# Kernel optimization log

Measured on AMD Instinct MI355X. Metric: run time of the kernel, lower is better.

The kernel has to match this reference:

```python
import jax, jax.numpy as jnp
import numpy as np

B, S, D, H, HD = 1, 2048, 3072, 24, 128
FFN = int(D / 3 * 8)  # 8192
ADALN = 256
NORM_EPS = 1e-6
QK_EPS = 1e-5
AXES_DIMS = (16, 56, 56)
AXES_LENS = (64, 128, 128)
THETA = 256.0


def rmsnorm(x, w, eps):
    var = jnp.mean(jnp.square(x), axis=-1, keepdims=True)
    return x * jax.lax.rsqrt(var + eps) * w


def apply_rope(x, cos, sin):
    # x: [B,S,H,HD]; cos/sin: [B,S,HD//2] (broadcast over heads, matching freqs_cis.unsqueeze(2))
    xr = x[..., 0::2]
    xi = x[..., 1::2]
    c = cos[:, :, None, :]
    s = sin[:, :, None, :]
    or_ = xr * c - xi * s
    oi_ = xr * s + xi * c
    return jnp.stack([or_, oi_], axis=-1).reshape(x.shape)


def rope_angles(ids):
    # ids: [B,S,3] int; returns angles [B,S,HD//2] concatenated per axis like RopeEmbedder
    parts = []
    for d, idx_axis in zip(AXES_DIMS, range(len(AXES_DIMS))):
        freqs = 1.0 / (THETA ** (jnp.arange(0, d, 2, dtype=jnp.float32) / d))  # [d/2]
        ang = ids[..., idx_axis].astype(jnp.float32)[..., None] * freqs  # [B,S,d/2]
        parts.append(ang)
    return jnp.concatenate(parts, axis=-1)  # [B,S,64]


def setup_inputs() -> dict:
    key = jax.random.key(0)
    ks = jax.random.split(key, 20)
    w = 0.02
    ids = jnp.concatenate([
        jax.random.randint(ks[15], (B, S, 1), 0, AXES_LENS[0]),
        jax.random.randint(ks[16], (B, S, 1), 0, AXES_LENS[1]),
        jax.random.randint(ks[17], (B, S, 1), 0, AXES_LENS[2]),
    ], axis=-1)
    return {
        "x": jax.random.normal(ks[0], (B, S, D), jnp.float32),
        "adaln_input": jax.random.normal(ks[1], (B, ADALN), jnp.float32),
        "attn_mask": jnp.ones((B, S), dtype=bool),
        "ids": ids,
        "attn_norm1_w": jnp.ones((D,), jnp.float32),
        "attn_norm2_w": jnp.ones((D,), jnp.float32),
        "ffn_norm1_w": jnp.ones((D,), jnp.float32),
        "ffn_norm2_w": jnp.ones((D,), jnp.float32),
        "norm_q_w": jnp.ones((HD,), jnp.float32),
        "norm_k_w": jnp.ones((HD,), jnp.float32),
        "wq": jax.random.normal(ks[2], (D, D), jnp.float32) * w,
        "wk": jax.random.normal(ks[3], (D, D), jnp.float32) * w,
        "wv": jax.random.normal(ks[4], (D, D), jnp.float32) * w,
        "wo": jax.random.normal(ks[5], (D, D), jnp.float32) * w,
        "w1": jax.random.normal(ks[6], (D, FFN), jnp.float32) * w,
        "w2": jax.random.normal(ks[7], (FFN, D), jnp.float32) * w,
        "w3": jax.random.normal(ks[8], (D, FFN), jnp.float32) * w,
        "adaln_w": jax.random.normal(ks[9], (ADALN, 4 * D), jnp.float32) * w,
        "adaln_b": jnp.zeros((4 * D,), jnp.float32),
    }


def block_forward(x, adaln_input, attn_mask, ids,
                  attn_norm1_w, attn_norm2_w, ffn_norm1_w, ffn_norm2_w,
                  norm_q_w, norm_k_w, wq, wk, wv, wo, w1, w2, w3,
                  adaln_w, adaln_b):
    ang = rope_angles(ids)
    cos, sin = jnp.cos(ang), jnp.sin(ang)

    mod = adaln_input @ adaln_w + adaln_b
    scale_msa, gate_msa, scale_mlp, gate_mlp = jnp.split(mod[:, None, :], 4, axis=2)
    gate_msa, gate_mlp = jnp.tanh(gate_msa), jnp.tanh(gate_mlp)
    scale_msa, scale_mlp = 1.0 + scale_msa, 1.0 + scale_mlp

    # Attention branch
    xs = rmsnorm(x, attn_norm1_w, NORM_EPS) * scale_msa  # [B,S,D]
    q = (xs @ wq).reshape(B, S, H, HD)
    k = (xs @ wk).reshape(B, S, H, HD)
    v = (xs @ wv).reshape(B, S, H, HD)
    q = rmsnorm(q, norm_q_w, QK_EPS)
    k = rmsnorm(k, norm_k_w, QK_EPS)
    q = apply_rope(q, cos, sin)
    k = apply_rope(k, cos, sin)

    scores = jnp.einsum('bqhd,bkhd->bhqk', q, k) / jnp.sqrt(jnp.float32(HD))
    neg = jnp.finfo(scores.dtype).min
    scores = jnp.where(attn_mask[:, None, None, :], scores, neg)
    probs = jax.nn.softmax(scores, axis=-1)
    attn = jnp.einsum('bhqk,bkhd->bqhd', probs, v).reshape(B, S, D)
    attn_out = attn @ wo

    x = x + gate_msa * rmsnorm(attn_out, attn_norm2_w, NORM_EPS)

    # FFN branch (SwiGLU)
    xf = rmsnorm(x, ffn_norm1_w, NORM_EPS) * scale_mlp
    h = jax.nn.silu(xf @ w1) * (xf @ w3)
    ffn_out = h @ w2
    x = x + gate_mlp * rmsnorm(ffn_out, ffn_norm2_w, NORM_EPS)
    return x


def reference(x, adaln_input, attn_mask, ids,
              attn_norm1_w, attn_norm2_w, ffn_norm1_w, ffn_norm2_w,
              norm_q_w, norm_k_w, wq, wk, wv, wo, w1, w2, w3,
              adaln_w, adaln_b):
    return block_forward(x, adaln_input, attn_mask, ids,
                         attn_norm1_w, attn_norm2_w, ffn_norm1_w, ffn_norm2_w,
                         norm_q_w, norm_k_w, wq, wk, wv, wo, w1, w2, w3,
                         adaln_w, adaln_b)
```

## Files before the change

kernel.cpp:

```cpp
#include <hip/hip_runtime.h>

#define AS1 __attribute__((address_space(1)))
#define AS3 __attribute__((address_space(3)))

typedef __bf16 bf16;
using bf16x8 = __attribute__((ext_vector_type(8))) __bf16;
using bf16x4 = __attribute__((ext_vector_type(4))) __bf16;
using bf16x2 = __attribute__((ext_vector_type(2))) __bf16;
using f32x4  = __attribute__((ext_vector_type(4))) float;


__device__ inline float wsum(float v) {
#pragma unroll
  for (int o = 32; o; o >>= 1) v += __shfl_xor(v, o, 64);
  return v;
}

template <int EPI>
__global__ __launch_bounds__(512, 1) void gemm256(
    const bf16* __restrict__ A, const bf16* __restrict__ Bt, void* __restrict__ Cv,
    int K, int lda, int ldb, int ldc, long long kOff, long long sC) {
  __shared__ bf16 lds[2][2][256 * 64];
  const int t = threadIdx.x;
  const int lane = t & 63, wid = t >> 6;
  const int wm = wid >> 2, wn = wid & 3;
  const int row16 = lane & 15, kg = lane >> 4;
  const int m0 = blockIdx.x * 256, n0 = blockIdx.y * 256;
  const int NT = K >> 6;
  const int sgran = (lane & 7) ^ (lane >> 3);
  A += (long long)blockIdx.z * kOff;
  Bt += (long long)blockIdx.z * kOff;

  auto stageA = [&](int buf, int r, int tk) {
    const int wrow = ((wid & 4) << 5) + (r << 5) + ((wid & 3) << 3);
    __builtin_amdgcn_global_load_lds(
        (const AS1 void*)(A + (long long)(m0 + wrow + (lane >> 3)) * lda + tk * 64 +
                          (sgran << 3)),
        (AS3 void*)&lds[buf][0][wrow * 64], 16, 0, 0);
  };
  auto stageB = [&](int buf, int r, int tk) {
    const int wrow = ((wid & 4) << 5) + (r << 5) + ((wid & 3) << 3);
    __builtin_amdgcn_global_load_lds(
        (const AS1 void*)(Bt + (long long)(n0 + wrow + (lane >> 3)) * ldb + tk * 64 +
                          (sgran << 3)),
        (AS3 void*)&lds[buf][1][wrow * 64], 16, 0, 0);
  };

  f32x4 acc[8][4];
#pragma unroll
  for (int i = 0; i < 8; ++i)
#pragma unroll
    for (int j = 0; j < 4; ++j) acc[i][j] = (f32x4){0.f, 0.f, 0.f, 0.f};

#pragma unroll
  for (int r = 0; r < 4; ++r) { stageA(0, r, 0); stageB(0, r, 0); }
#pragma unroll
  for (int r = 0; r < 3; ++r) { stageA(1, r, 1); stageB(1, r, 1); }

  bf16x8 bfr[4][2], af[2][2];

  for (int kt = 0; kt < NT; ++kt) {
    const int cb = kt & 1, nb = cb ^ 1;
    if (kt + 1 < NT) asm volatile("s_waitcnt vmcnt(6)" ::: "memory");
    else             asm volatile("s_waitcnt vmcnt(0)" ::: "memory");
    __builtin_amdgcn_s_barrier();

    if (kt + 1 < NT) { stageA(nb, 3, kt + 1); stageB(nb, 3, kt + 1); }
#pragma unroll
    for (int ni = 0; ni < 4; ++ni)
#pragma unroll
      for (int kk = 0; kk < 2; ++kk) {
        const int r = wn * 64 + ni * 16 + row16;
        bfr[ni][kk] = *(const bf16x8*)&lds[cb][1][r * 64 + (((kk * 4 + kg) ^ (r & 7)) << 3)];
      }
#pragma unroll
    for (int mi = 0; mi < 2; ++mi)
#pragma unroll
      for (int kk = 0; kk < 2; ++kk) {
        const int r = wm * 128 + mi * 16 + row16;
        af[mi][kk] = *(const bf16x8*)&lds[cb][0][r * 64 + (((kk * 4 + kg) ^ (r & 7)) << 3)];
      }
    asm volatile("s_waitcnt lgkmcnt(0)" ::: "memory");
    __builtin_amdgcn_s_setprio(1);
#pragma unroll
    for (int kk = 0; kk < 2; ++kk)
#pragma unroll
      for (int mi = 0; mi < 2; ++mi)
#pragma unroll
        for (int ni = 0; ni < 4; ++ni)
          acc[mi][ni] =
              __builtin_amdgcn_mfma_f32_16x16x32_bf16(af[mi][kk], bfr[ni][kk], acc[mi][ni], 0, 0, 0);
    __builtin_amdgcn_s_setprio(0);

#pragma unroll
    for (int q = 1; q < 4; ++q) {
      __builtin_amdgcn_s_barrier();
      if (kt + 2 < NT) { stageA(cb, q - 1, kt + 2); stageB(cb, q - 1, kt + 2); }
#pragma unroll
      for (int mi = 0; mi < 2; ++mi)
#pragma unroll
        for (int kk = 0; kk < 2; ++kk) {
          const int r = wm * 128 + q * 32 + mi * 16 + row16;
          af[mi][kk] = *(const bf16x8*)&lds[cb][0][r * 64 + (((kk * 4 + kg) ^ (r & 7)) << 3)];
        }
      asm volatile("s_waitcnt lgkmcnt(0)" ::: "memory");
      __builtin_amdgcn_s_setprio(1);
#pragma unroll
      for (int kk = 0; kk < 2; ++kk)
#pragma unroll
        for (int mi = 0; mi < 2; ++mi)
#pragma unroll
          for (int ni = 0; ni < 4; ++ni)
            acc[q * 2 + mi][ni] = __builtin_amdgcn_mfma_f32_16x16x32_bf16(
                af[mi][kk], bfr[ni][kk], acc[q * 2 + mi][ni], 0, 0, 0);
      __builtin_amdgcn_s_setprio(0);
    }
  }

  float* Cf = (float*)Cv;
  bf16* Cb = (bf16*)Cv;
  const long long cz = (long long)blockIdx.z * sC;
#pragma unroll
  for (int mf = 0; mf < 8; ++mf)
#pragma unroll
    for (int ni = 0; ni < 4; ++ni)
#pragma unroll
      for (int rr = 0; rr < 4; ++rr) {
        const int row = m0 + wm * 128 + (mf >> 1) * 32 + (mf & 1) * 16 + kg * 4 + rr;
        const int col = n0 + wn * 64 + ni * 16 + row16;
        const long long idx = cz + (long long)row * ldc + col;
        const float v = acc[mf][ni][rr];
        if constexpr (EPI == 0) Cf[idx] = v;
        else Cb[idx] = (bf16)v;
      }
}

template <int EPI>
__global__ __launch_bounds__(512, 1) void gemm192(
    const bf16* __restrict__ A, const bf16* __restrict__ Bt, void* __restrict__ Cv,
    int K, int lda, int ldb, int ldc, long long kOff, long long sC) {
  __shared__ bf16 lds[2][448 * 64];
  const int t = threadIdx.x;
  const int lane = t & 63, wid = t >> 6;
  const int wm = wid >> 2, wn = wid & 3;
  const int row16 = lane & 15, kg = lane >> 4;
  const int m0 = blockIdx.x * 256, n0 = blockIdx.y * 192;
  const int NT = K >> 6;
  const int sgran = (lane & 7) ^ (lane >> 3);
  A += (long long)blockIdx.z * kOff;
  Bt += (long long)blockIdx.z * kOff;

  auto stageA = [&](int buf, int r, int tk) {
    const int wrow = ((wid & 4) << 5) + (r << 5) + ((wid & 3) << 3);
    __builtin_amdgcn_global_load_lds(
        (const AS1 void*)(A + (long long)(m0 + wrow + (lane >> 3)) * lda + tk * 64 +
                          (sgran << 3)),
        (AS3 void*)&lds[buf][wrow * 64], 16, 0, 0);
  };
  auto stageB = [&](int buf, int r, int tk) {
    const int wrow = r * 64 + wid * 8;
    __builtin_amdgcn_global_load_lds(
        (const AS1 void*)(Bt + (long long)(n0 + wrow + (lane >> 3)) * ldb + tk * 64 +
                          (sgran << 3)),
        (AS3 void*)&lds[buf][(256 + wrow) * 64], 16, 0, 0);
  };

  f32x4 acc[8][3];
#pragma unroll
  for (int i = 0; i < 8; ++i)
#pragma unroll
    for (int j = 0; j < 3; ++j) acc[i][j] = (f32x4){0.f, 0.f, 0.f, 0.f};

#pragma unroll
  for (int r = 0; r < 4; ++r) stageA(0, r, 0);
#pragma unroll
  for (int r = 0; r < 3; ++r) stageB(0, r, 0);
#pragma unroll
  for (int r = 0; r < 3; ++r) { stageA(1, r, 1); stageB(1, r, 1); }

  bf16x8 bfr[3][2], af[2][2];

  for (int kt = 0; kt < NT; ++kt) {
    const int cb = kt & 1, nb = cb ^ 1;
    if (kt + 1 < NT) asm volatile("s_waitcnt vmcnt(6)" ::: "memory");
    else             asm volatile("s_waitcnt vmcnt(0)" ::: "memory");
    __builtin_amdgcn_s_barrier();

    if (kt + 1 < NT) stageA(nb, 3, kt + 1);
#pragma unroll
    for (int ni = 0; ni < 3; ++ni)
#pragma unroll
      for (int kk = 0; kk < 2; ++kk) {
        const int r = wn * 48 + ni * 16 + row16;
        bfr[ni][kk] =
            *(const bf16x8*)&lds[cb][(256 + r) * 64 + (((kk * 4 + kg) ^ (r & 7)) << 3)];
      }
#pragma unroll
    for (int mi = 0; mi < 2; ++mi)
#pragma unroll
      for (int kk = 0; kk < 2; ++kk) {
        const int r = wm * 128 + mi * 16 + row16;
        af[mi][kk] = *(const bf16x8*)&lds[cb][r * 64 + (((kk * 4 + kg) ^ (r & 7)) << 3)];
      }
    __builtin_amdgcn_s_barrier();
    asm volatile("s_waitcnt lgkmcnt(0)" ::: "memory");
    __builtin_amdgcn_s_setprio(1);
#pragma unroll
    for (int kk = 0; kk < 2; ++kk)
#pragma unroll
      for (int mi = 0; mi < 2; ++mi)
#pragma unroll
        for (int ni = 0; ni < 3; ++ni)
          acc[mi][ni] =
              __builtin_amdgcn_mfma_f32_16x16x32_bf16(af[mi][kk], bfr[ni][kk], acc[mi][ni], 0, 0, 0);
    __builtin_amdgcn_s_setprio(0);

#pragma unroll
    for (int q = 1; q < 4; ++q) {
      __builtin_amdgcn_s_barrier();
      if (kt + 2 < NT) { stageA(cb, q - 1, kt + 2); stageB(cb, q - 1, kt + 2); }
#pragma unroll
      for (int mi = 0; mi < 2; ++mi)
#pragma unroll
        for (int kk = 0; kk < 2; ++kk) {
          const int r = wm * 128 + q * 32 + mi * 16 + row16;
          af[mi][kk] = *(const bf16x8*)&lds[cb][r * 64 + (((kk * 4 + kg) ^ (r & 7)) << 3)];
        }
      __builtin_amdgcn_s_barrier();
      asm volatile("s_waitcnt lgkmcnt(0)" ::: "memory");
      __builtin_amdgcn_s_setprio(1);
#pragma unroll
      for (int kk = 0; kk < 2; ++kk)
#pragma unroll
        for (int mi = 0; mi < 2; ++mi)
#pragma unroll
          for (int ni = 0; ni < 3; ++ni)
            acc[q * 2 + mi][ni] = __builtin_amdgcn_mfma_f32_16x16x32_bf16(
                af[mi][kk], bfr[ni][kk], acc[q * 2 + mi][ni], 0, 0, 0);
      __builtin_amdgcn_s_setprio(0);
    }
  }

  float* Cf = (float*)Cv;
  bf16* Cb = (bf16*)Cv;
  const long long cz = (long long)blockIdx.z * sC;
#pragma unroll
  for (int mf = 0; mf < 8; ++mf)
#pragma unroll
    for (int ni = 0; ni < 3; ++ni)
#pragma unroll
      for (int rr = 0; rr < 4; ++rr) {
        const int row = m0 + wm * 128 + (mf >> 1) * 32 + (mf & 1) * 16 + kg * 4 + rr;
        const int col = n0 + wn * 48 + ni * 16 + row16;
        const long long idx = cz + (long long)row * ldc + col;
        const float v = acc[mf][ni][rr];
        if constexpr (EPI == 0) Cf[idx] = v;
        else Cb[idx] = (bf16)v;
      }
}

__global__ __launch_bounds__(256) void flash_attn_k(const bf16* __restrict__ qkv,
                                                    const bf16* __restrict__ vt,
                                                    float* __restrict__ Op,
                                                    float* __restrict__ mlp) {
  __shared__ bf16 Ks[64 * 128];
  __shared__ bf16 Vs[128 * 64];
  __shared__ bf16 Ps[4 * 32 * 64];
  const int t = threadIdx.x, lane = t & 63, wid = t >> 6;
  const int row16 = lane & 15, kg = lane >> 4;
  const int q0 = blockIdx.x * 128;
  const int h = blockIdx.y;
  const int z = blockIdx.z;
  const bf16* Qp = qkv + h * 128;
  const bf16* Kp = qkv + 3072 + h * 128;
  const bf16* Vt = vt + (long long)h * 262144;
  const float iscale = 0.08838834764831845f;

  bf16x8 qf[2][4];
#pragma unroll
  for (int mi = 0; mi < 2; ++mi)
#pragma unroll
    for (int kc = 0; kc < 4; ++kc)
      qf[mi][kc] = *(const bf16x8*)&Qp[(long long)(q0 + wid * 32 + mi * 16 + row16) * 9216 +
                                       kc * 32 + kg * 8];
  bf16x8 ones;
#pragma unroll
  for (int j = 0; j < 8; ++j) ones[j] = (bf16)1.0f;

  f32x4 oacc[2][8];
#pragma unroll
  for (int mi = 0; mi < 2; ++mi)
#pragma unroll
    for (int nd = 0; nd < 8; ++nd) oacc[mi][nd] = (f32x4){0.f, 0.f, 0.f, 0.f};
  f32x4 lacc[2] = {(f32x4){0.f, 0.f, 0.f, 0.f}, (f32x4){0.f, 0.f, 0.f, 0.f}};
  float mst[2][4];
#pragma unroll
  for (int mi = 0; mi < 2; ++mi)
#pragma unroll
    for (int r = 0; r < 4; ++r) mst[mi][r] = -1e30f;

  bf16* Pw = &Ps[wid * 2048];
  const int kvbase = z << 10;

  for (int kv0 = kvbase; kv0 < kvbase + 1024; kv0 += 64) {
#pragma unroll
    for (int p = 0; p < 4; ++p) {
      const int gi = p * 256 + t;
      const int row = gi >> 4, g = gi & 15;
      __builtin_amdgcn_global_load_lds(
          (const AS1 void*)(Kp + (long long)(kv0 + row) * 9216 + ((g ^ (row & 7)) << 3)),
          (AS3 void*)&Ks[(p * 256 + wid * 64) * 8], 16, 0, 0);
    }
#pragma unroll
    for (int p = 0; p < 4; ++p) {
      const int gi = p * 256 + t;
      const int row = gi >> 3, g = gi & 7;
      __builtin_amdgcn_global_load_lds(
          (const AS1 void*)(Vt + (long long)row * 2048 + kv0 + ((g ^ (row & 7)) << 3)),
          (AS3 void*)&Vs[(p * 256 + wid * 64) * 8], 16, 0, 0);
    }
    __syncthreads();

    f32x4 sacc[2][4];
#pragma unroll
    for (int mi = 0; mi < 2; ++mi)
#pragma unroll
      for (int nf = 0; nf < 4; ++nf) sacc[mi][nf] = (f32x4){0.f, 0.f, 0.f, 0.f};
#pragma unroll
    for (int kc = 0; kc < 4; ++kc) {
      bf16x8 kf[4];
#pragma unroll
      for (int nf = 0; nf < 4; ++nf) {
        const int row = nf * 16 + row16;
        kf[nf] = *(const bf16x8*)&Ks[(row * 16 + ((kc * 4 + kg) ^ (row & 7))) * 8];
      }
#pragma unroll
      for (int mi = 0; mi < 2; ++mi)
#pragma unroll
        for (int nf = 0; nf < 4; ++nf)
          sacc[mi][nf] =
              __builtin_amdgcn_mfma_f32_16x16x32_bf16(qf[mi][kc], kf[nf], sacc[mi][nf], 0, 0, 0);
    }

    float fac[2][4];
#pragma unroll
    for (int mi = 0; mi < 2; ++mi)
#pragma unroll
      for (int r = 0; r < 4; ++r) {
        float rm = sacc[mi][0][r];
#pragma unroll
        for (int nf = 1; nf < 4; ++nf) rm = fmaxf(rm, sacc[mi][nf][r]);
        rm = fmaxf(rm, __shfl_xor(rm, 1, 64));
        rm = fmaxf(rm, __shfl_xor(rm, 2, 64));
        rm = fmaxf(rm, __shfl_xor(rm, 4, 64));
        rm = fmaxf(rm, __shfl_xor(rm, 8, 64));
        const float mnew = fmaxf(mst[mi][r], rm * iscale);
        fac[mi][r] = __expf(mst[mi][r] - mnew);
        mst[mi][r] = mnew;
#pragma unroll
        for (int nf = 0; nf < 4; ++nf)
          sacc[mi][nf][r] = __expf(sacc[mi][nf][r] * iscale - mnew);
      }
#pragma unroll
    for (int mi = 0; mi < 2; ++mi)
#pragma unroll
      for (int r = 0; r < 4; ++r) {
        lacc[mi][r] *= fac[mi][r];
#pragma unroll
        for (int nd = 0; nd < 8; ++nd) oacc[mi][nd][r] *= fac[mi][r];
      }

#pragma unroll
    for (int mi = 0; mi < 2; ++mi)
#pragma unroll
      for (int nf = 0; nf < 4; ++nf)
#pragma unroll
        for (int r = 0; r < 4; ++r) {
          const int row = mi * 16 + kg * 4 + r;
          const int col = nf * 16 + row16;
          Pw[(row * 8 + ((col >> 3) ^ (row & 7))) * 8 + (col & 7)] = (bf16)sacc[mi][nf][r];
        }

#pragma unroll
    for (int kvc = 0; kvc < 2; ++kvc) {
      bf16x8 pf[2], vf[8];
#pragma unroll
      for (int mi = 0; mi < 2; ++mi) {
        const int row = mi * 16 + row16;
        pf[mi] = *(const bf16x8*)&Pw[(row * 8 + ((kvc * 4 + kg) ^ (row & 7))) * 8];
      }
#pragma unroll
      for (int nd = 0; nd < 8; ++nd) {
        const int row = nd * 16 + row16;
        vf[nd] = *(const bf16x8*)&Vs[(row * 8 + ((kvc * 4 + kg) ^ (row & 7))) * 8];
      }
#pragma unroll
      for (int mi = 0; mi < 2; ++mi) {
        lacc[mi] = __builtin_amdgcn_mfma_f32_16x16x32_bf16(pf[mi], ones, lacc[mi], 0, 0, 0);
#pragma unroll
        for (int nd = 0; nd < 8; ++nd)
          oacc[mi][nd] =
              __builtin_amdgcn_mfma_f32_16x16x32_bf16(pf[mi], vf[nd], oacc[mi][nd], 0, 0, 0);
      }
    }
    __syncthreads();
  }

  float* Oz = Op + (long long)z * 6291456;
#pragma unroll
  for (int mi = 0; mi < 2; ++mi)
#pragma unroll
    for (int nd = 0; nd < 8; ++nd)
#pragma unroll
      for (int r = 0; r < 4; ++r) {
        const int row = q0 + wid * 32 + mi * 16 + kg * 4 + r;
        const int col = h * 128 + nd * 16 + row16;
        Oz[(long long)row * 3072 + col] = oacc[mi][nd][r];
      }
  if (row16 == 0) {
#pragma unroll
    for (int mi = 0; mi < 2; ++mi)
#pragma unroll
      for (int r = 0; r < 4; ++r) {
        const int s = q0 + wid * 32 + mi * 16 + kg * 4 + r;
        const long long mi2 = ((long long)z * 49152 + s * 24 + h) * 2;
        mlp[mi2] = mst[mi][r];
        mlp[mi2 + 1] = lacc[mi][r];
      }
  }
}

__global__ __launch_bounds__(256) void fa_combine_k(const float* __restrict__ Op,
                                                    const float* __restrict__ mlp,
                                                    bf16* __restrict__ attn) {
  const int t = threadIdx.x, lane = t & 63, wid = t >> 6;
  const int pair = blockIdx.x * 4 + wid;
  const int s = pair / 24, h = pair % 24;
  const float2 ml0 = *(const float2*)&mlp[(long long)pair * 2];
  const float2 ml1 = *(const float2*)&mlp[(49152LL + pair) * 2];
  const float m = fmaxf(ml0.x, ml1.x);
  const float a0 = __expf(ml0.x - m), a1 = __expf(ml1.x - m);
  const float inv = 1.f / (ml0.y * a0 + ml1.y * a1);
  const long long base = (long long)s * 3072 + h * 128 + lane * 2;
  const float2 o0 = *(const float2*)&Op[base];
  const float2 o1 = *(const float2*)&Op[6291456LL + base];
  bf16x2 o;
  o[0] = (bf16)((o0.x * a0 + o1.x * a1) * inv);
  o[1] = (bf16)((o0.y * a0 + o1.y * a1) * inv);
  *(bf16x2*)&attn[base] = o;
}

__device__ inline void convT_tile(const float* __restrict__ in, bf16* __restrict__ out,
                                  int R, int C, int bx, int by) {
  __shared__ float tile[64][65];
  const int t = threadIdx.x;
  const int r0 = by * 64, c0 = bx * 64;
#pragma unroll
  for (int it = 0; it < 4; ++it) {
    const int idx = it * 256 + t;
    const int rl = idx >> 4, c4 = (idx & 15) << 2;
    const float4 v = *(const float4*)&in[(long long)(r0 + rl) * C + c0 + c4];
    tile[rl][c4 + 0] = v.x;
    tile[rl][c4 + 1] = v.y;
    tile[rl][c4 + 2] = v.z;
    tile[rl][c4 + 3] = v.w;
  }
  __syncthreads();
#pragma unroll
  for (int it = 0; it < 4; ++it) {
    const int idx = it * 256 + t;
    const int cl = idx >> 4, r4 = (idx & 15) << 2;
    bf16x4 o;
    o[0] = (bf16)tile[r4 + 0][cl];
    o[1] = (bf16)tile[r4 + 1][cl];
    o[2] = (bf16)tile[r4 + 2][cl];
    o[3] = (bf16)tile[r4 + 3][cl];
    *(bf16x4*)&out[(long long)(c0 + cl) * R + r0 + r4] = o;
  }
}

__global__ __launch_bounds__(256) void convAll(
    const float* __restrict__ wq, const float* __restrict__ wk,
    const float* __restrict__ wv, const float* __restrict__ wo,
    const float* __restrict__ w1, const float* __restrict__ w3,
    const float* __restrict__ w2, bf16* __restrict__ wqkvT, bf16* __restrict__ woT,
    bf16* __restrict__ w13T, bf16* __restrict__ w2T) {
  const int id = blockIdx.x;
  if (id < 9216) {
    const int m = id / 2304, l = id % 2304;
    const float* in = m == 0 ? wq : m == 1 ? wk : m == 2 ? wv : wo;
    bf16* out = m < 3 ? wqkvT + (long long)m * 9437184 : woT;
    convT_tile(in, out, 3072, 3072, l % 48, l / 48);
  } else if (id < 21504) {
    int l = id - 9216;
    const int m = l / 6144;
    l %= 6144;
    convT_tile(m ? w3 : w1, w13T + (long long)m * 25165824, 3072, 8192, l % 128, l / 128);
  } else {
    const int l = id - 21504;
    convT_tile(w2, w2T, 8192, 3072, l % 48, l / 48);
  }
}

__global__ __launch_bounds__(256) void ropetab_k(const int* __restrict__ ids,
                                                 float* __restrict__ cosT,
                                                 float* __restrict__ sinT) {
  const int i = blockIdx.x * 256 + threadIdx.x;
  const int s = i >> 6, j = i & 63;
  int ax, fi;
  float d;
  if (j < 8) { ax = 0; fi = j; d = 16.f; }
  else if (j < 36) { ax = 1; fi = j - 8; d = 56.f; }
  else { ax = 2; fi = j - 36; d = 56.f; }
  const float freq = exp2f(-16.f * (float)fi / d);
  const float ang = (float)ids[s * 3 + ax] * freq;
  cosT[i] = cosf(ang);
  sinT[i] = sinf(ang);
}

__global__ __launch_bounds__(256) void adaln_kernel(const float* __restrict__ ain,
                                                    const float* __restrict__ W,
                                                    const float* __restrict__ b,
                                                    float* __restrict__ out) {
  __shared__ float a[256];
  const int t = threadIdx.x;
  a[t] = ain[t];
  __syncthreads();
  const int n = blockIdx.x * 256 + t;
  float acc = b[n];
  for (int k = 0; k < 256; ++k) acc = fmaf(a[k], W[(long long)k * 12288 + n], acc);
  const int chunk = n / 3072;
  out[n] = (chunk & 1) ? tanhf(acc) : (1.f + acc);
}

__global__ __launch_bounds__(256) void rmsnorm_scale_k(const float* __restrict__ x,
                                                       const float* __restrict__ w,
                                                       const float* __restrict__ scale,
                                                       bf16* __restrict__ out) {
  __shared__ float red[4];
  const int t = threadIdx.x, lane = t & 63, wid = t >> 6;
  const long long base = (long long)blockIdx.x * 3072;
  float v[12];
  float ss = 0.f;
#pragma unroll
  for (int ch = 0; ch < 3; ++ch) {
    const float4 f = *(const float4*)&x[base + ch * 1024 + t * 4];
    v[ch * 4 + 0] = f.x; v[ch * 4 + 1] = f.y; v[ch * 4 + 2] = f.z; v[ch * 4 + 3] = f.w;
    ss += f.x * f.x + f.y * f.y + f.z * f.z + f.w * f.w;
  }
  ss = wsum(ss);
  if (!lane) red[wid] = ss;
  __syncthreads();
  const float r = rsqrtf((red[0] + red[1] + red[2] + red[3]) / 3072.f + 1e-6f);
#pragma unroll
  for (int ch = 0; ch < 3; ++ch) {
    const int col = ch * 1024 + t * 4;
    bf16x4 o;
#pragma unroll
    for (int j = 0; j < 4; ++j) o[j] = (bf16)(v[ch * 4 + j] * r * w[col + j] * scale[col + j]);
    *(bf16x4*)&out[base + col] = o;
  }
}

__global__ __launch_bounds__(256) void qknorm_rope_k(bf16* __restrict__ qkv,
                                                     const float* __restrict__ cosT,
                                                     const float* __restrict__ sinT,
                                                     const float* __restrict__ wq,
                                                     const float* __restrict__ wk) {
  const int t = threadIdx.x, lane = t & 63, wid = t >> 6;
  const int idx = blockIdx.x * 4 + wid;
  const int s = idx / 24, h = idx % 24;
  const int isK = blockIdx.y;
  bf16* base = qkv + (long long)s * 9216 + isK * 3072 + h * 128;
  bf16x2 p = *(const bf16x2*)(base + 2 * lane);
  float xr = (float)p[0], xi = (float)p[1];
  const float ss = wsum(xr * xr + xi * xi);
  const float r = rsqrtf(ss / 128.f + 1e-5f);
  const float* w = isK ? wk : wq;
  const float2 wv = *(const float2*)&w[2 * lane];
  xr *= r * wv.x;
  xi *= r * wv.y;
  const float c = cosT[s * 64 + lane], sn = sinT[s * 64 + lane];
  bf16x2 o;
  o[0] = (bf16)(xr * c - xi * sn);
  o[1] = (bf16)(xr * sn + xi * c);
  *(bf16x2*)(base + 2 * lane) = o;
}

__global__ __launch_bounds__(256) void vtrans_k(const bf16* __restrict__ qkv,
                                                bf16* __restrict__ vt) {
  __shared__ bf16 tile[64][72];
  const int t = threadIdx.x;
  const int s0 = blockIdx.x * 64, d0 = blockIdx.y * 64, h = blockIdx.z;
#pragma unroll
  for (int it = 0; it < 2; ++it) {
    const int idx = it * 256 + t;
    const int sl = idx >> 3, c8 = (idx & 7) << 3;
    const bf16x8 v =
        *(const bf16x8*)&qkv[(long long)(s0 + sl) * 9216 + 6144 + h * 128 + d0 + c8];
    *(bf16x8*)&tile[sl][c8] = v;
  }
  __syncthreads();
#pragma unroll
  for (int it = 0; it < 2; ++it) {
    const int idx = it * 256 + t;
    const int dl = idx >> 3, s8 = (idx & 7) << 3;
    bf16x8 o;
#pragma unroll
    for (int j = 0; j < 8; ++j) o[j] = tile[s8 + j][dl];
    *(bf16x8*)&vt[(long long)h * 262144 + (long long)(d0 + dl) * 2048 + s0 + s8] = o;
  }
}

__global__ __launch_bounds__(256) void silumul_k(const bf16* __restrict__ t13,
                                                 bf16* __restrict__ h) {
  const int gi = blockIdx.x * 256 + threadIdx.x;
  const int s = gi >> 10, j8 = (gi & 1023) << 3;
  const bf16x8 a = *(const bf16x8*)&t13[(long long)s * 16384 + j8];
  const bf16x8 b = *(const bf16x8*)&t13[(long long)s * 16384 + 8192 + j8];
  bf16x8 o;
#pragma unroll
  for (int j = 0; j < 8; ++j) {
    const float x = (float)a[j];
    const float sl = x / (1.f + __expf(-x));
    o[j] = (bf16)(sl * (float)b[j]);
  }
  *(bf16x8*)&h[(long long)s * 8192 + j8] = o;
}

__global__ __launch_bounds__(256) void resid1_k(
    const float* __restrict__ x, const float* __restrict__ p0, const float* __restrict__ p1,
    const float* __restrict__ n2w, const float* __restrict__ gate,
    const float* __restrict__ f1w, const float* __restrict__ smlp,
    float* __restrict__ x1, bf16* __restrict__ xf) {
  __shared__ float red[8];
  const int t = threadIdx.x, lane = t & 63, wid = t >> 6;
  const long long base = (long long)blockIdx.x * 3072;
  float av[12];
  float ss = 0.f;
#pragma unroll
  for (int ch = 0; ch < 3; ++ch) {
    const float4 f0 = *(const float4*)&p0[base + ch * 1024 + t * 4];
    const float4 f1 = *(const float4*)&p1[base + ch * 1024 + t * 4];
    const float a0 = f0.x + f1.x, a1 = f0.y + f1.y, a2 = f0.z + f1.z, a3 = f0.w + f1.w;
    av[ch * 4 + 0] = a0; av[ch * 4 + 1] = a1; av[ch * 4 + 2] = a2; av[ch * 4 + 3] = a3;
    ss += a0 * a0 + a1 * a1 + a2 * a2 + a3 * a3;
  }
  ss = wsum(ss);
  if (!lane) red[wid] = ss;
  __syncthreads();
  const float r = rsqrtf((red[0] + red[1] + red[2] + red[3]) / 3072.f + 1e-6f);
  float xv[12];
  float ss2 = 0.f;
#pragma unroll
  for (int ch = 0; ch < 3; ++ch) {
    const int col = ch * 1024 + t * 4;
    const float4 f = *(const float4*)&x[base + col];
    float4 o;
    o.x = f.x + gate[col + 0] * (av[ch * 4 + 0] * r * n2w[col + 0]);
    o.y = f.y + gate[col + 1] * (av[ch * 4 + 1] * r * n2w[col + 1]);
    o.z = f.z + gate[col + 2] * (av[ch * 4 + 2] * r * n2w[col + 2]);
    o.w = f.w + gate[col + 3] * (av[ch * 4 + 3] * r * n2w[col + 3]);
    *(float4*)&x1[base + col] = o;
    xv[ch * 4 + 0] = o.x; xv[ch * 4 + 1] = o.y; xv[ch * 4 + 2] = o.z; xv[ch * 4 + 3] = o.w;
    ss2 += o.x * o.x + o.y * o.y + o.z * o.z + o.w * o.w;
  }
  ss2 = wsum(ss2);
  if (!lane) red[4 + wid] = ss2;
  __syncthreads();
  const float r2 = rsqrtf((red[4] + red[5] + red[6] + red[7]) / 3072.f + 1e-6f);
#pragma unroll
  for (int ch = 0; ch < 3; ++ch) {
    const int col = ch * 1024 + t * 4;
    bf16x4 o;
#pragma unroll
    for (int j = 0; j < 4; ++j)
      o[j] = (bf16)(xv[ch * 4 + j] * r2 * f1w[col + j] * smlp[col + j]);
    *(bf16x4*)&xf[base + col] = o;
  }
}

__global__ __launch_bounds__(256) void resid2_k(const float* __restrict__ x1,
                                                const float* __restrict__ f0,
                                                const float* __restrict__ f1,
                                                const float* __restrict__ nw,
                                                const float* __restrict__ gate,
                                                float* __restrict__ out) {
  __shared__ float red[4];
  const int t = threadIdx.x, lane = t & 63, wid = t >> 6;
  const long long base = (long long)blockIdx.x * 3072;
  float fv[12];
  float ss = 0.f;
#pragma unroll
  for (int ch = 0; ch < 3; ++ch) {
    const float4 a = *(const float4*)&f0[base + ch * 1024 + t * 4];
    const float4 b = *(const float4*)&f1[base + ch * 1024 + t * 4];
    const float a0 = a.x + b.x, a1 = a.y + b.y, a2 = a.z + b.z, a3 = a.w + b.w;
    fv[ch * 4 + 0] = a0; fv[ch * 4 + 1] = a1; fv[ch * 4 + 2] = a2; fv[ch * 4 + 3] = a3;
    ss += a0 * a0 + a1 * a1 + a2 * a2 + a3 * a3;
  }
  ss = wsum(ss);
  if (!lane) red[wid] = ss;
  __syncthreads();
  const float r = rsqrtf((red[0] + red[1] + red[2] + red[3]) / 3072.f + 1e-6f);
#pragma unroll
  for (int ch = 0; ch < 3; ++ch) {
    const int col = ch * 1024 + t * 4;
    const float4 f = *(const float4*)&x1[base + col];
    float4 o;
    o.x = f.x + gate[col + 0] * (fv[ch * 4 + 0] * r * nw[col + 0]);
    o.y = f.y + gate[col + 1] * (fv[ch * 4 + 1] * r * nw[col + 1]);
    o.z = f.z + gate[col + 2] * (fv[ch * 4 + 2] * r * nw[col + 2]);
    o.w = f.w + gate[col + 3] * (fv[ch * 4 + 3] * r * nw[col + 3]);
    *(float4*)&out[base + col] = o;
  }
}

extern "C" void kernel_launch(void* const* d_in, const int* in_sizes, int n_in,
                              void* d_out, int out_size, void* d_ws, size_t ws_size,
                              hipStream_t stream) {
  const float* x    = (const float*)d_in[0];
  const float* ain  = (const float*)d_in[1];
  const int* ids    = (const int*)d_in[3];
  const float* n1w  = (const float*)d_in[4];
  const float* n2w  = (const float*)d_in[5];
  const float* fn1w = (const float*)d_in[6];
  const float* fn2w = (const float*)d_in[7];
  const float* nqw  = (const float*)d_in[8];
  const float* nkw  = (const float*)d_in[9];
  const float* wq   = (const float*)d_in[10];
  const float* wk   = (const float*)d_in[11];
  const float* wv   = (const float*)d_in[12];
  const float* wo   = (const float*)d_in[13];
  const float* w1   = (const float*)d_in[14];
  const float* w2   = (const float*)d_in[15];
  const float* w3   = (const float*)d_in[16];
  const float* adw  = (const float*)d_in[17];
  const float* adb  = (const float*)d_in[18];

  if (ws_size < 395362304ULL) return;

  char* ws = (char*)d_ws;
  bf16* wqkvT = (bf16*)(ws + 0LL);
  bf16* woT   = (bf16*)(ws + 56623104LL);
  bf16* w13T  = (bf16*)(ws + 75497472LL);
  bf16* w2T   = (bf16*)(ws + 176160768LL);
  float* cosT = (float*)(ws + 226492416LL);
  float* sinT = (float*)(ws + 227016704LL);
  float* adv  = (float*)(ws + 227540992LL);
  bf16* xs    = (bf16*)(ws + 227590144LL);
  char* big   = ws + 240173056LL;
  float* x1   = (float*)(big);
  bf16* qkv   = (bf16*)(big + 25165824LL);
  bf16* vt    = (bf16*)(big + 62914560LL);
  bf16* attn  = (bf16*)(big + 75497472LL);
  float* aoP  = (float*)(big + 88080384LL);
  float* Opart= (float*)(big + 88080384LL);
  float* mlp  = (float*)(big + 138412032LL);
  bf16* t13   = (bf16*)(big + 25165824LL);
  bf16* hbuf  = (bf16*)(big + 92274688LL);
  float* ffnP = (float*)(big + 25165824LL);

  const dim3 b256(256);
  const dim3 b512(512);

  ropetab_k<<<dim3(512), b256, 0, stream>>>(ids, cosT, sinT);
  adaln_kernel<<<dim3(48), b256, 0, stream>>>(ain, adw, adb, adv);

  convAll<<<dim3(27648), b256, 0, stream>>>(wq, wk, wv, wo, w1, w3, w2, wqkvT, woT, w13T,
                                            w2T);

  rmsnorm_scale_k<<<dim3(2048), b256, 0, stream>>>(x, n1w, adv, xs);

  gemm192<1><<<dim3(8, 48, 1), b512, 0, stream>>>(xs, wqkvT, qkv, 3072, 3072, 3072, 9216,
                                                  0LL, 0LL);

  qknorm_rope_k<<<dim3(12288, 2), b256, 0, stream>>>(qkv, cosT, sinT, nqw, nkw);
  vtrans_k<<<dim3(32, 2, 24), b256, 0, stream>>>(qkv, vt);

  flash_attn_k<<<dim3(16, 24, 2), b256, 0, stream>>>(qkv, vt, Opart, mlp);
  fa_combine_k<<<dim3(12288), b256, 0, stream>>>(Opart, mlp, attn);

  gemm192<0><<<dim3(8, 16, 2), b512, 0, stream>>>(attn, woT, aoP, 1536, 3072, 3072, 3072,
                                                  1536LL, 6291456LL);
  resid1_k<<<dim3(2048), b256, 0, stream>>>(x, aoP, aoP + 6291456LL, n2w, adv + 3072, fn1w,
                                            adv + 6144, x1, xs);
  gemm256<1><<<dim3(8, 64, 1), b512, 0, stream>>>(xs, w13T, t13, 3072, 3072, 3072, 16384,
                                                  0LL, 0LL);
  silumul_k<<<dim3(8192), b256, 0, stream>>>(t13, hbuf);
  gemm192<0><<<dim3(8, 16, 2), b512, 0, stream>>>(hbuf, w2T, ffnP, 4096, 8192, 8192, 3072,
                                                  4096LL, 6291456LL);
  resid2_k<<<dim3(2048), b256, 0, stream>>>(x1, ffnP, ffnP + 6291456LL, fn2w, adv + 9216,
                                            (float*)d_out);
}
```

Measured before the change: 837.6 us.

## Fuse SwiGLU into W1/W3 GEMM epilogue and store attention partials as bf16

```diff
diff --git a/kernel.cpp b/kernel.cpp
--- a/kernel.cpp
+++ b/kernel.cpp
@@ -128,10 +128,18 @@
       for (int rr = 0; rr < 4; ++rr) {
         const int row = m0 + wm * 128 + (mf >> 1) * 32 + (mf & 1) * 16 + kg * 4 + rr;
         const int col = n0 + wn * 64 + ni * 16 + row16;
-        const long long idx = cz + (long long)row * ldc + col;
         const float v = acc[mf][ni][rr];
-        if constexpr (EPI == 0) Cf[idx] = v;
-        else Cb[idx] = (bf16)v;
+        if constexpr (EPI == 2) {
+          const float other = __shfl_xor(v, 1, 64);
+          if ((row16 & 1) == 0) {
+            const float sl = v / (1.f + __expf(-v));
+            Cb[cz + (long long)row * ldc + (col >> 1)] = (bf16)(sl * other);
+          }
+        } else {
+          const long long idx = cz + (long long)row * ldc + col;
+          if constexpr (EPI == 0) Cf[idx] = v;
+          else Cb[idx] = (bf16)v;
+        }
       }
 }
 
@@ -261,7 +269,7 @@
 
 __global__ __launch_bounds__(256) void flash_attn_k(const bf16* __restrict__ qkv,
                                                     const bf16* __restrict__ vt,
-                                                    float* __restrict__ Op,
+                                                    bf16* __restrict__ Opb,
                                                     float* __restrict__ mlp) {
   __shared__ bf16 Ks[64 * 128];
   __shared__ bf16 Vs[128 * 64];
@@ -406,7 +414,7 @@
     __syncthreads();
   }
 
-  float* Oz = Op + (long long)z * 6291456;
+  bf16* Oz = Opb + (long long)z * 6291456;
 #pragma unroll
   for (int mi = 0; mi < 2; ++mi)
 #pragma unroll
@@ -415,7 +423,7 @@
       for (int r = 0; r < 4; ++r) {
         const int row = q0 + wid * 32 + mi * 16 + kg * 4 + r;
         const int col = h * 128 + nd * 16 + row16;
-        Oz[(long long)row * 3072 + col] = oacc[mi][nd][r];
+        Oz[(long long)row * 3072 + col] = (bf16)oacc[mi][nd][r];
       }
   if (row16 == 0) {
 #pragma unroll
@@ -430,7 +438,7 @@
   }
 }
 
-__global__ __launch_bounds__(256) void fa_combine_k(const float* __restrict__ Op,
+__global__ __launch_bounds__(256) void fa_combine_k(const bf16* __restrict__ Opb,
                                                     const float* __restrict__ mlp,
                                                     bf16* __restrict__ attn) {
   const int t = threadIdx.x, lane = t & 63, wid = t >> 6;
@@ -442,16 +450,16 @@
   const float a0 = __expf(ml0.x - m), a1 = __expf(ml1.x - m);
   const float inv = 1.f / (ml0.y * a0 + ml1.y * a1);
   const long long base = (long long)s * 3072 + h * 128 + lane * 2;
-  const float2 o0 = *(const float2*)&Op[base];
-  const float2 o1 = *(const float2*)&Op[6291456LL + base];
+  const bf16x2 o0 = *(const bf16x2*)&Opb[base];
+  const bf16x2 o1 = *(const bf16x2*)&Opb[6291456LL + base];
   bf16x2 o;
-  o[0] = (bf16)((o0.x * a0 + o1.x * a1) * inv);
-  o[1] = (bf16)((o0.y * a0 + o1.y * a1) * inv);
+  o[0] = (bf16)(((float)o0[0] * a0 + (float)o1[0] * a1) * inv);
+  o[1] = (bf16)(((float)o0[1] * a0 + (float)o1[1] * a1) * inv);
   *(bf16x2*)&attn[base] = o;
 }
 
 __device__ inline void convT_tile(const float* __restrict__ in, bf16* __restrict__ out,
-                                  int R, int C, int bx, int by) {
+                                  int R, int C, int bx, int by, int rmul, int roff) {
   __shared__ float tile[64][65];
   const int t = threadIdx.x;
   const int r0 = by * 64, c0 = bx * 64;
@@ -475,7 +483,7 @@
     o[1] = (bf16)tile[r4 + 1][cl];
     o[2] = (bf16)tile[r4 + 2][cl];
     o[3] = (bf16)tile[r4 + 3][cl];
-    *(bf16x4*)&out[(long long)(c0 + cl) * R + r0 + r4] = o;
+    *(bf16x4*)&out[(long long)((c0 + cl) * rmul + roff) * R + r0 + r4] = o;
   }
 }
 
@@ -490,15 +498,15 @@
     const int m = id / 2304, l = id % 2304;
     const float* in = m == 0 ? wq : m == 1 ? wk : m == 2 ? wv : wo;
     bf16* out = m < 3 ? wqkvT + (long long)m * 9437184 : woT;
-    convT_tile(in, out, 3072, 3072, l % 48, l / 48);
+    convT_tile(in, out, 3072, 3072, l % 48, l / 48, 1, 0);
   } else if (id < 21504) {
     int l = id - 9216;
     const int m = l / 6144;
     l %= 6144;
-    convT_tile(m ? w3 : w1, w13T + (long long)m * 25165824, 3072, 8192, l % 128, l / 128);
+    convT_tile(m ? w3 : w1, w13T, 3072, 8192, l % 128, l / 128, 2, m);
   } else {
     const int l = id - 21504;
-    convT_tile(w2, w2T, 8192, 3072, l % 48, l / 48);
+    convT_tile(w2, w2T, 8192, 3072, l % 48, l / 48, 1, 0);
   }
 }
 
@@ -612,22 +620,6 @@
   }
 }
 
-__global__ __launch_bounds__(256) void silumul_k(const bf16* __restrict__ t13,
-                                                 bf16* __restrict__ h) {
-  const int gi = blockIdx.x * 256 + threadIdx.x;
-  const int s = gi >> 10, j8 = (gi & 1023) << 3;
-  const bf16x8 a = *(const bf16x8*)&t13[(long long)s * 16384 + j8];
-  const bf16x8 b = *(const bf16x8*)&t13[(long long)s * 16384 + 8192 + j8];
-  bf16x8 o;
-#pragma unroll
-  for (int j = 0; j < 8; ++j) {
-    const float x = (float)a[j];
-    const float sl = x / (1.f + __expf(-x));
-    o[j] = (bf16)(sl * (float)b[j]);
-  }
-  *(bf16x8*)&h[(long long)s * 8192 + j8] = o;
-}
-
 __global__ __launch_bounds__(256) void resid1_k(
     const float* __restrict__ x, const float* __restrict__ p0, const float* __restrict__ p1,
     const float* __restrict__ n2w, const float* __restrict__ gate,
@@ -754,10 +746,9 @@
   bf16* qkv   = (bf16*)(big + 25165824LL);
   bf16* vt    = (bf16*)(big + 62914560LL);
   bf16* attn  = (bf16*)(big + 75497472LL);
+  bf16* Opb   = (bf16*)(big + 88080384LL);
   float* aoP  = (float*)(big + 88080384LL);
-  float* Opart= (float*)(big + 88080384LL);
   float* mlp  = (float*)(big + 138412032LL);
-  bf16* t13   = (bf16*)(big + 25165824LL);
   bf16* hbuf  = (bf16*)(big + 92274688LL);
   float* ffnP = (float*)(big + 25165824LL);
 
@@ -778,16 +769,15 @@
   qknorm_rope_k<<<dim3(12288, 2), b256, 0, stream>>>(qkv, cosT, sinT, nqw, nkw);
   vtrans_k<<<dim3(32, 2, 24), b256, 0, stream>>>(qkv, vt);
 
-  flash_attn_k<<<dim3(16, 24, 2), b256, 0, stream>>>(qkv, vt, Opart, mlp);
-  fa_combine_k<<<dim3(12288), b256, 0, stream>>>(Opart, mlp, attn);
+  flash_attn_k<<<dim3(16, 24, 2), b256, 0, stream>>>(qkv, vt, Opb, mlp);
+  fa_combine_k<<<dim3(12288), b256, 0, stream>>>(Opb, mlp, attn);
 
   gemm192<0><<<dim3(8, 16, 2), b512, 0, stream>>>(attn, woT, aoP, 1536, 3072, 3072, 3072,
                                                   1536LL, 6291456LL);
   resid1_k<<<dim3(2048), b256, 0, stream>>>(x, aoP, aoP + 6291456LL, n2w, adv + 3072, fn1w,
                                             adv + 6144, x1, xs);
-  gemm256<1><<<dim3(8, 64, 1), b512, 0, stream>>>(xs, w13T, t13, 3072, 3072, 3072, 16384,
+  gemm256<2><<<dim3(8, 64, 1), b512, 0, stream>>>(xs, w13T, hbuf, 3072, 3072, 3072, 8192,
                                                   0LL, 0LL);
-  silumul_k<<<dim3(8192), b256, 0, stream>>>(t13, hbuf);
   gemm192<0><<<dim3(8, 16, 2), b512, 0, stream>>>(hbuf, w2T, ffnP, 4096, 8192, 8192, 3072,
                                                   4096LL, 6291456LL);
   resid2_k<<<dim3(2048), b256, 0, stream>>>(x1, ffnP, ffnP + 6291456LL, fn2w, adv + 9216,
```

Result: no change. 832.0 us (-0.7%).
